# Kernel optimization log

Hardware: AMD Instinct MI355X
Metric: run time of the kernel (lower is better)

The kernel has to match this reference:

```python
import jax, jax.numpy as jnp
import numpy as np

B, H, W, C = 16, 56, 56, 256
NH, WS, SS = 8, 7, 3          # heads, window size, shift size
HD = C // NH                  # head dim = 32
MLPD = 4 * C                  # mlp hidden = 1024
WA = WS * WS                  # window area = 49
NW = (H // WS) * (W // WS)    # windows per image = 64
SCALE = HD ** -0.5


def _rel_pos_index():
    coords = np.stack(np.meshgrid(np.arange(WS), np.arange(WS), indexing='ij'))
    cf = coords.reshape(2, -1)
    rel = (cf[:, :, None] - cf[:, None, :]).transpose(1, 2, 0)
    rel[:, :, 0] += WS - 1
    rel[:, :, 1] += WS - 1
    rel[:, :, 0] *= 2 * WS - 1
    return rel.sum(-1)  # (WA, WA) int


def _shift_attn_mask():
    img = np.zeros((H, W))
    cnt = 0
    for hs in (slice(0, -WS), slice(-WS, -SS), slice(-SS, None)):
        for ws_ in (slice(0, -WS), slice(-WS, -SS), slice(-SS, None)):
            img[hs, ws_] = cnt
            cnt += 1
    mw = img.reshape(H // WS, WS, W // WS, WS).transpose(0, 2, 1, 3).reshape(-1, WA)
    am = mw[:, None, :] - mw[:, :, None]
    return np.where(am != 0, -100.0, 0.0).astype(np.float32)  # (NW, WA, WA)

REL_IDX = jnp.asarray(_rel_pos_index())
ATTN_MASK = jnp.asarray(_shift_attn_mask())


def setup_inputs() -> dict:
    key = jax.random.key(0)
    ks = jax.random.split(key, 8)
    s = 0.02
    return {
        'x':      jax.random.normal(ks[0], (B, H * W, C), jnp.float32),
        'g1':     jnp.ones((C,), jnp.float32),
        'be1':    jnp.zeros((C,), jnp.float32),
        'w_qkv':  jax.random.normal(ks[1], (C, 3 * C), jnp.float32) * s,
        'b_qkv':  jnp.zeros((3 * C,), jnp.float32),
        'rpt':    jax.random.normal(ks[2], ((2 * WS - 1) ** 2, NH), jnp.float32) * s,
        'w_proj': jax.random.normal(ks[3], (C, C), jnp.float32) * s,
        'b_proj': jnp.zeros((C,), jnp.float32),
        'g2':     jnp.ones((C,), jnp.float32),
        'be2':    jnp.zeros((C,), jnp.float32),
        'w_fc1':  jax.random.normal(ks[4], (C, MLPD), jnp.float32) * s,
        'b_fc1':  jnp.zeros((MLPD,), jnp.float32),
        'w_fc2':  jax.random.normal(ks[5], (MLPD, C), jnp.float32) * s,
        'b_fc2':  jnp.zeros((C,), jnp.float32),
    }


def _ln(x, g, b, eps=1e-5):
    m = x.mean(-1, keepdims=True)
    v = ((x - m) ** 2).mean(-1, keepdims=True)
    return (x - m) * jax.lax.rsqrt(v + eps) * g + b


def reference(x, g1, be1, w_qkv, b_qkv, rpt, w_proj, b_proj, g2, be2,
              w_fc1, b_fc1, w_fc2, b_fc2):
    shortcut = x
    h = _ln(x, g1, be1).reshape(B, H, W, C)
    # cyclic shift
    h = jnp.roll(h, (-SS, -SS), axis=(1, 2))
    # window partition -> (B*NW, WA, C)
    h = h.reshape(B, H // WS, WS, W // WS, WS, C).transpose(0, 1, 3, 2, 4, 5)
    h = h.reshape(B * NW, WA, C)
    # qkv
    qkv = h @ w_qkv + b_qkv                       # (B*NW, WA, 3C)
    qkv = qkv.reshape(B * NW, WA, 3, NH, HD).transpose(2, 0, 3, 1, 4)
    q, k, v = qkv[0], qkv[1], qkv[2]              # (B*NW, NH, WA, HD)
    attn = jnp.einsum('wnqd,wnkd->wnqk', q * SCALE, k)   # (B*NW, NH, WA, WA)
    # relative position bias
    bias = rpt[REL_IDX.reshape(-1)].reshape(WA, WA, NH).transpose(2, 0, 1)
    attn = attn + bias[None]
    # shifted-window mask, per window
    attn = attn.reshape(B, NW, NH, WA, WA) + ATTN_MASK[None, :, None]
    attn = jax.nn.softmax(attn.reshape(B * NW, NH, WA, WA), axis=-1)
    out = jnp.einsum('wnqk,wnkd->wnqd', attn, v)  # (B*NW, NH, WA, HD)
    out = out.transpose(0, 2, 1, 3).reshape(B * NW, WA, C)
    out = out @ w_proj + b_proj
    # window reverse + unshift
    out = out.reshape(B, H // WS, W // WS, WS, WS, C).transpose(0, 1, 3, 2, 4, 5)
    out = out.reshape(B, H, W, C)
    out = jnp.roll(out, (SS, SS), axis=(1, 2)).reshape(B, H * W, C)
    x = shortcut + out
    # MLP block
    h2 = _ln(x, g2, be2)
    h2 = jax.nn.gelu(h2 @ w_fc1 + b_fc1, approximate=False) @ w_fc2 + b_fc2
    return x + h2
```

## Files before the change

kernel.cpp:

```cpp
#include <hip/hip_runtime.h>
#include <hip/hip_bf16.h>
#include <cstdint>
#include <cstddef>

typedef __attribute__((ext_vector_type(8))) short short8;
typedef __attribute__((ext_vector_type(4))) float f32x4;
typedef __attribute__((ext_vector_type(4))) unsigned short us4;

#define DEVINL __device__ __forceinline__

static constexpr int SS_ = 3;
static constexpr int HH = 56, WW = 56;
#define SCALE_Q 0.17677669529663689f

DEVINL unsigned short f2b(float f) {
    unsigned int u = __builtin_bit_cast(unsigned int, f);
    unsigned int r = (u + 0x7FFFu + ((u >> 16) & 1u)) >> 16;
    return (unsigned short)r;
}
DEVINL float b2f(unsigned short s) {
    return __builtin_bit_cast(float, ((unsigned int)s) << 16);
}

DEVINL void gload_lds16(const unsigned short* g, unsigned short* l) {
    __builtin_amdgcn_global_load_lds(
        (const __attribute__((address_space(1))) unsigned int*)g,
        (__attribute__((address_space(3))) unsigned int*)l, 16, 0, 0);
}

__global__ void wconv_kernel(const float* __restrict__ in,
                             unsigned short* __restrict__ out, int K, int N) {
    int i = blockIdx.x * 256 + threadIdx.x;
    if (i >= K * N) return;
    int k = i / N, n = i - k * N;
    out[(size_t)n * K + k] = f2b(in[i]);
}

template <int MODE>
__global__ __launch_bounds__(256) void ln_kernel(
    const float* __restrict__ x, const float* __restrict__ g,
    const float* __restrict__ be, unsigned short* __restrict__ out) {
    const int wid = threadIdx.x >> 6, lane = threadIdx.x & 63;
    const int t = blockIdx.x * 4 + wid;
    int src;
    if constexpr (MODE == 1) {
        int w = t / 49, p = t - w * 49;
        int b = w >> 6, widx = w & 63;
        int wy = widx >> 3, wx = widx & 7;
        int py = p / 7, px = p - py * 7;
        int y = wy * 7 + py + SS_;  if (y >= HH) y -= HH;
        int xx = wx * 7 + px + SS_; if (xx >= WW) xx -= WW;
        src = b * (HH * WW) + y * WW + xx;
    } else {
        src = t;
    }
    const float4 v = reinterpret_cast<const float4*>(x + (size_t)src * 256)[lane];
    float s = v.x + v.y + v.z + v.w;
    float q = v.x * v.x + v.y * v.y + v.z * v.z + v.w * v.w;
#pragma unroll
    for (int m = 1; m < 64; m <<= 1) {
        s += __shfl_xor(s, m);
        q += __shfl_xor(q, m);
    }
    float mean = s * (1.0f / 256.0f);
    float var = q * (1.0f / 256.0f) - mean * mean;
    float rs = rsqrtf(var + 1e-5f);
    int c = lane * 4;
    us4 o;
    o.x = f2b((v.x - mean) * rs * g[c + 0] + be[c + 0]);
    o.y = f2b((v.y - mean) * rs * g[c + 1] + be[c + 1]);
    o.z = f2b((v.z - mean) * rs * g[c + 2] + be[c + 2]);
    o.w = f2b((v.w - mean) * rs * g[c + 3] + be[c + 3]);
    *reinterpret_cast<us4*>(out + (size_t)t * 256 + c) = o;
}

template <int KDIM, int EPI>
__global__ __launch_bounds__(512) void gemm_kernel(
    const unsigned short* __restrict__ A, const unsigned short* __restrict__ Bt,
    const float* __restrict__ bias, void* __restrict__ out0,
    const float* __restrict__ res, unsigned short* __restrict__ o_q,
    unsigned short* __restrict__ o_k, unsigned short* __restrict__ o_v) {
    constexpr int BM = 256, BN = 128, BK = 64;
    __shared__ __align__(16) unsigned short As[BM * BK];
    __shared__ __align__(16) unsigned short Bs[BN * BK];
    const int tid = threadIdx.x;
    const int wid = tid >> 6, lane = tid & 63;

    const int nwg = gridDim.x * gridDim.y;
    const int bid = blockIdx.x + gridDim.x * blockIdx.y;
    const int nb = (bid & 7) * (nwg >> 3) + (bid >> 3);
    const int n0 = (nb % gridDim.x) * BN;
    const int m0 = (nb / gridDim.x) * BM;

    const int wm = wid >> 1, wn = wid & 1;
    const int lr = lane & 15, kg = lane >> 4;
    f32x4 acc[4][4] = {};

    const int srow = tid >> 3;
    const int spos = tid & 7;

    for (int kt = 0; kt < KDIM; kt += BK) {
#pragma unroll
        for (int i = 0; i < 4; i++) {
            int row = i * 64 + srow;
            gload_lds16(A + (size_t)(m0 + row) * KDIM + kt + ((spos ^ (row & 7)) << 3),
                        As + i * 4096 + tid * 8);
        }
#pragma unroll
        for (int i = 0; i < 2; i++) {
            int row = i * 64 + srow;
            gload_lds16(Bt + (size_t)(n0 + row) * KDIM + kt + ((spos ^ (row & 7)) << 3),
                        Bs + i * 4096 + tid * 8);
        }
        __syncthreads();
#pragma unroll
        for (int ks = 0; ks < 2; ks++) {
            short8 a[4], b[4];
#pragma unroll
            for (int mf = 0; mf < 4; mf++) {
                int r = wm * 64 + mf * 16 + lr;
                a[mf] = *reinterpret_cast<const short8*>(
                    As + r * 64 + (((ks * 4 + kg) ^ (r & 7)) << 3));
            }
#pragma unroll
            for (int nf = 0; nf < 4; nf++) {
                int r = wn * 64 + nf * 16 + lr;
                b[nf] = *reinterpret_cast<const short8*>(
                    Bs + r * 64 + (((ks * 4 + kg) ^ (r & 7)) << 3));
            }
#pragma unroll
            for (int mf = 0; mf < 4; mf++)
#pragma unroll
                for (int nf = 0; nf < 4; nf++)
                    acc[mf][nf] = __builtin_amdgcn_mfma_f32_16x16x32_bf16(
                        a[mf], b[nf], acc[mf][nf], 0, 0, 0);
        }
        __syncthreads();
    }

#pragma unroll
    for (int mf = 0; mf < 4; mf++) {
#pragma unroll
        for (int nf = 0; nf < 4; nf++) {
#pragma unroll
            for (int j = 0; j < 4; j++) {
                int row = m0 + wm * 64 + mf * 16 + kg * 4 + j;
                int col = n0 + wn * 64 + nf * 16 + lr;
                float v = acc[mf][nf][j] + bias[col];
                if constexpr (EPI == 0) {
                    int w = row / 49, p = row - w * 49;
                    int which = col >> 8, h = (col >> 5) & 7, d = col & 31;
                    size_t th = (size_t)(w * 8 + h);
                    if (which == 0)
                        o_q[th * 1568 + p * 32 + d] = f2b(v * SCALE_Q);
                    else if (which == 1)
                        o_k[th * 1568 + p * 32 + d] = f2b(v);
                    else
                        o_v[th * 2048 + d * 64 + p] = f2b(v);
                } else if constexpr (EPI == 1) {
                    int w = row / 49, p = row - w * 49;
                    int b = w >> 6, widx = w & 63;
                    int wy = widx >> 3, wx = widx & 7;
                    int py = p / 7, px = p - py * 7;
                    int y = wy * 7 + py + SS_;  if (y >= HH) y -= HH;
                    int xx = wx * 7 + px + SS_; if (xx >= WW) xx -= WW;
                    size_t oi = ((size_t)(b * 3136 + y * 56 + xx)) * 256 + col;
                    reinterpret_cast<float*>(out0)[oi] = v + res[oi];
                } else if constexpr (EPI == 2) {
                    float gl = 0.5f * v * (1.0f + erff(v * 0.70710678118654752f));
                    reinterpret_cast<unsigned short*>(out0)[(size_t)row * 1024 + col] =
                        f2b(gl);
                } else {
                    size_t oi = (size_t)row * 256 + col;
                    reinterpret_cast<float*>(out0)[oi] = v + res[oi];
                }
            }
        }
    }
}

__global__ __launch_bounds__(256) void attn_kernel(
    const unsigned short* __restrict__ qg, const unsigned short* __restrict__ kgl,
    const unsigned short* __restrict__ vg, const float* __restrict__ rpt,
    unsigned short* __restrict__ out) {
    __shared__ __align__(16) unsigned short sm[4][6144];
    __shared__ unsigned short rpts[169 * 8];
    const int tid = threadIdx.x, wid = tid >> 6, lane = tid & 63;
    for (int i = tid; i < 169 * 8; i += 256) rpts[i] = f2b(rpt[i]);
    const int task = blockIdx.x * 4 + wid;
    const int w = task >> 3, h = task & 7;
    const int widx = w & 63, wy = widx >> 3, wx = widx & 7;
    unsigned short* q_s = sm[wid];
    unsigned short* k_s = sm[wid] + 2048;
    unsigned short* v_s = sm[wid] + 4096;
    unsigned short* p_s = sm[wid];
    const unsigned short* qsrc = qg + (size_t)task * 1568;
    const unsigned short* ksrc = kgl + (size_t)task * 1568;
    const unsigned short* vsrc = vg + (size_t)task * 2048;
    for (int c = lane; c < 196; c += 64) {
        int row = c >> 2, kc = c & 3;
        int off = (row * 32 + kc * 8) ^ ((row & 7) << 3);
        *reinterpret_cast<short8*>(q_s + off) =
            *reinterpret_cast<const short8*>(qsrc + c * 8);
        *reinterpret_cast<short8*>(k_s + off) =
            *reinterpret_cast<const short8*>(ksrc + c * 8);
    }
#pragma unroll
    for (int i = 0; i < 4; i++) {
        int c = i * 64 + lane;
        int row = c >> 3, kc = c & 7;
        int off = (row * 64 + kc * 8) ^ ((row & 7) << 3);
        *reinterpret_cast<short8*>(v_s + off) =
            *reinterpret_cast<const short8*>(vsrc + c * 8);
    }
    __syncthreads();

    const int lr = lane & 15, kg = lane >> 4;
    short8 af[4], bf[4];
#pragma unroll
    for (int mf = 0; mf < 4; mf++) {
        int r = mf * 16 + lr;
        af[mf] = *reinterpret_cast<const short8*>(
            q_s + ((r * 32 + kg * 8) ^ ((r & 7) << 3)));
    }
#pragma unroll
    for (int nf = 0; nf < 4; nf++) {
        int r = nf * 16 + lr;
        bf[nf] = *reinterpret_cast<const short8*>(
            k_s + ((r * 32 + kg * 8) ^ ((r & 7) << 3)));
    }
    f32x4 s[4][4] = {};
#pragma unroll
    for (int mf = 0; mf < 4; mf++)
#pragma unroll
        for (int nf = 0; nf < 4; nf++)
            s[mf][nf] = __builtin_amdgcn_mfma_f32_16x16x32_bf16(af[mf], bf[nf],
                                                                s[mf][nf], 0, 0, 0);
#pragma unroll
    for (int mf = 0; mf < 4; mf++) {
#pragma unroll
        for (int j = 0; j < 4; j++) {
            int row = mf * 16 + kg * 4 + j;
            bool rvalid = row < 49;
            int qy = 0, qx = 0, gq = 0;
            if (rvalid) {
                qy = row / 7; qx = row - qy * 7;
                int yi = wy * 7 + qy, xi = wx * 7 + qx;
                gq = ((yi < 49) ? 0 : ((yi < 53) ? 1 : 2)) * 3 +
                     ((xi < 49) ? 0 : ((xi < 53) ? 1 : 2));
            }
            float L[4];
#pragma unroll
            for (int nf = 0; nf < 4; nf++) {
                int col = nf * 16 + lr;
                float val = s[mf][nf][j];
                if (rvalid && col < 49) {
                    int ky = col / 7, kx = col - ky * 7;
                    int yi = wy * 7 + ky, xi = wx * 7 + kx;
                    int gk = ((yi < 49) ? 0 : ((yi < 53) ? 1 : 2)) * 3 +
                             ((xi < 49) ? 0 : ((xi < 53) ? 1 : 2));
                    val += b2f(rpts[((qy - ky + 6) * 13 + (qx - kx + 6)) * 8 + h]);
                    if (gq != gk) val -= 100.0f;
                } else {
                    val = -1e30f;
                }
                L[nf] = val;
            }
            float m = fmaxf(fmaxf(L[0], L[1]), fmaxf(L[2], L[3]));
#pragma unroll
            for (int t2 = 1; t2 < 16; t2 <<= 1) m = fmaxf(m, __shfl_xor(m, t2));
            float P[4], psum = 0.f;
#pragma unroll
            for (int nf = 0; nf < 4; nf++) {
                P[nf] = __expf(L[nf] - m);
                psum += P[nf];
            }
#pragma unroll
            for (int t2 = 1; t2 < 16; t2 <<= 1) psum += __shfl_xor(psum, t2);
            float inv = 1.0f / psum;
#pragma unroll
            for (int nf = 0; nf < 4; nf++) {
                int col = nf * 16 + lr;
                p_s[(row * 64 + col) ^ ((row & 7) << 3)] = f2b(P[nf] * inv);
            }
        }
    }
    f32x4 o[4][2] = {};
#pragma unroll
    for (int ks = 0; ks < 2; ks++) {
        short8 pa[4], vb[2];
#pragma unroll
        for (int mf = 0; mf < 4; mf++) {
            int r = mf * 16 + lr;
            pa[mf] = *reinterpret_cast<const short8*>(
                p_s + ((r * 64 + ks * 32 + kg * 8) ^ ((r & 7) << 3)));
        }
#pragma unroll
        for (int nf = 0; nf < 2; nf++) {
            int d = nf * 16 + lr;
            vb[nf] = *reinterpret_cast<const short8*>(
                v_s + ((d * 64 + ks * 32 + kg * 8) ^ ((d & 7) << 3)));
        }
#pragma unroll
        for (int mf = 0; mf < 4; mf++)
#pragma unroll
            for (int nf = 0; nf < 2; nf++)
                o[mf][nf] = __builtin_amdgcn_mfma_f32_16x16x32_bf16(
                    pa[mf], vb[nf], o[mf][nf], 0, 0, 0);
    }
#pragma unroll
    for (int mf = 0; mf < 4; mf++) {
#pragma unroll
        for (int j = 0; j < 4; j++) {
            int row = mf * 16 + kg * 4 + j;
            if (row < 49) {
#pragma unroll
                for (int nf = 0; nf < 2; nf++) {
                    int d = nf * 16 + lr;
                    out[((size_t)w * 49 + row) * 256 + h * 32 + d] =
                        f2b(o[mf][nf][j]);
                }
            }
        }
    }
}

extern "C" void kernel_launch(void* const* d_in, const int* in_sizes, int n_in,
                              void* d_out, int out_size, void* d_ws,
                              size_t ws_size, hipStream_t stream) {
    const float* x     = (const float*)d_in[0];
    const float* g1    = (const float*)d_in[1];
    const float* be1   = (const float*)d_in[2];
    const float* wqkv  = (const float*)d_in[3];
    const float* bqkv  = (const float*)d_in[4];
    const float* rpt   = (const float*)d_in[5];
    const float* wproj = (const float*)d_in[6];
    const float* bproj = (const float*)d_in[7];
    const float* g2    = (const float*)d_in[8];
    const float* be2   = (const float*)d_in[9];
    const float* wfc1  = (const float*)d_in[10];
    const float* bfc1  = (const float*)d_in[11];
    const float* wfc2  = (const float*)d_in[12];
    const float* bfc2  = (const float*)d_in[13];
    float* out = (float*)d_out;
    char* ws = (char*)d_ws;

    unsigned short* hb  = (unsigned short*)(ws);
    unsigned short* qg  = (unsigned short*)(ws + 25690112);
    unsigned short* kgl = (unsigned short*)(ws + 51380224);
    unsigned short* vg  = (unsigned short*)(ws + 77070336);
    float*          x2  = (float*)(ws + 110624768);
    unsigned short* h2  = (unsigned short*)(ws + 162004992);
    unsigned short* wT  = (unsigned short*)(ws + 187695104);
    unsigned short* wqkvT = wT;
    unsigned short* wprojT = wT + 196608;
    unsigned short* wfc1T  = wT + 262144;
    unsigned short* wfc2T  = wT + 524288;
    unsigned short* a1 = (unsigned short*)ws;

    wconv_kernel<<<(256 * 768 + 255) / 256, 256, 0, stream>>>(wqkv, wqkvT, 256, 768);
    wconv_kernel<<<(256 * 256 + 255) / 256, 256, 0, stream>>>(wproj, wprojT, 256, 256);
    wconv_kernel<<<(256 * 1024 + 255) / 256, 256, 0, stream>>>(wfc1, wfc1T, 256, 1024);
    wconv_kernel<<<(1024 * 256 + 255) / 256, 256, 0, stream>>>(wfc2, wfc2T, 1024, 256);
    hipMemsetAsync(vg, 0, 33554432, stream);

    ln_kernel<1><<<12544, 256, 0, stream>>>(x, g1, be1, hb);
    gemm_kernel<256, 0><<<dim3(6, 196), 512, 0, stream>>>(
        hb, wqkvT, bqkv, nullptr, nullptr, qg, kgl, vg);
    attn_kernel<<<2048, 256, 0, stream>>>(qg, kgl, vg, rpt, hb);
    gemm_kernel<256, 1><<<dim3(2, 196), 512, 0, stream>>>(
        hb, wprojT, bproj, x2, x, nullptr, nullptr, nullptr);
    ln_kernel<0><<<12544, 256, 0, stream>>>(x2, g2, be2, h2);
    gemm_kernel<256, 2><<<dim3(8, 196), 512, 0, stream>>>(
        h2, wfc1T, bfc1, a1, nullptr, nullptr, nullptr, nullptr);
    gemm_kernel<1024, 3><<<dim3(2, 196), 512, 0, stream>>>(
        a1, wfc2T, bfc2, out, x2, nullptr, nullptr, nullptr);
}
```

Baseline: 320.3 us.

## Double-buffer GEMM loads, store residual in bf16, approximate GELU, drop V memset

The GEMM main loop now uses BK=32 with two LDS buffers and a new swizzle, so the next tile's global-to-LDS load overlaps the current MFMAs and one barrier per iteration is removed. The intermediate residual x2 is written and read as bf16 instead of fp32, halving that tensor's traffic, at some cost in precision. GELU switches from erff to an Abramowitz-Stegun polynomial with __expf. The memset of the padded V buffer is removed; this is only safe if the attention kernel never reads the padding, which is a correctness risk.

```diff
diff --git a/kernel.cpp b/kernel.cpp
--- a/kernel.cpp
+++ b/kernel.cpp
@@ -2,6 +2,7 @@
 #include <hip/hip_bf16.h>
 #include <cstdint>
 #include <cstddef>
+#include <type_traits>
 
 typedef __attribute__((ext_vector_type(8))) short short8;
 typedef __attribute__((ext_vector_type(4))) float f32x4;
@@ -20,6 +21,19 @@
 }
 DEVINL float b2f(unsigned short s) {
     return __builtin_bit_cast(float, ((unsigned int)s) << 16);
+}
+
+DEVINL float gelu(float v) {
+    float ax = fabsf(v) * 0.70710678118654752f;
+    float t = 1.0f / (1.0f + 0.3275911f * ax);
+    float poly = t * (0.254829592f +
+                 t * (-0.284496736f +
+                 t * (1.421413741f +
+                 t * (-1.453152027f + t * 1.061405429f))));
+    float e = __expf(-ax * ax);
+    float erfv = 1.0f - poly * e;
+    erfv = v >= 0.0f ? erfv : -erfv;
+    return 0.5f * v * (1.0f + erfv);
 }
 
 DEVINL void gload_lds16(const unsigned short* g, unsigned short* l) {
@@ -36,9 +50,9 @@
     out[(size_t)n * K + k] = f2b(in[i]);
 }
 
-template <int MODE>
+template <int MODE, typename TIN>
 __global__ __launch_bounds__(256) void ln_kernel(
-    const float* __restrict__ x, const float* __restrict__ g,
+    const TIN* __restrict__ x, const float* __restrict__ g,
     const float* __restrict__ be, unsigned short* __restrict__ out) {
     const int wid = threadIdx.x >> 6, lane = threadIdx.x & 63;
     const int t = blockIdx.x * 4 + wid;
@@ -54,7 +68,13 @@
     } else {
         src = t;
     }
-    const float4 v = reinterpret_cast<const float4*>(x + (size_t)src * 256)[lane];
+    float4 v;
+    if constexpr (std::is_same_v<TIN, float>) {
+        v = reinterpret_cast<const float4*>(x + (size_t)src * 256)[lane];
+    } else {
+        us4 u = reinterpret_cast<const us4*>(x + (size_t)src * 256)[lane];
+        v.x = b2f(u.x); v.y = b2f(u.y); v.z = b2f(u.z); v.w = b2f(u.w);
+    }
     float s = v.x + v.y + v.z + v.w;
     float q = v.x * v.x + v.y * v.y + v.z * v.z + v.w * v.w;
 #pragma unroll
@@ -78,11 +98,11 @@
 __global__ __launch_bounds__(512) void gemm_kernel(
     const unsigned short* __restrict__ A, const unsigned short* __restrict__ Bt,
     const float* __restrict__ bias, void* __restrict__ out0,
-    const float* __restrict__ res, unsigned short* __restrict__ o_q,
+    const void* __restrict__ res, unsigned short* __restrict__ o_q,
     unsigned short* __restrict__ o_k, unsigned short* __restrict__ o_v) {
-    constexpr int BM = 256, BN = 128, BK = 64;
-    __shared__ __align__(16) unsigned short As[BM * BK];
-    __shared__ __align__(16) unsigned short Bs[BN * BK];
+    constexpr int BM = 256, BN = 128, BK = 32, NK = KDIM / BK;
+    __shared__ __align__(16) unsigned short As[2][BM * BK];
+    __shared__ __align__(16) unsigned short Bs[2][BN * BK];
     const int tid = threadIdx.x;
     const int wid = tid >> 6, lane = tid & 63;
 
@@ -96,46 +116,50 @@
     const int lr = lane & 15, kg = lane >> 4;
     f32x4 acc[4][4] = {};
 
-    const int srow = tid >> 3;
-    const int spos = tid & 7;
-
-    for (int kt = 0; kt < KDIM; kt += BK) {
-#pragma unroll
-        for (int i = 0; i < 4; i++) {
-            int row = i * 64 + srow;
-            gload_lds16(A + (size_t)(m0 + row) * KDIM + kt + ((spos ^ (row & 7)) << 3),
-                        As + i * 4096 + tid * 8);
-        }
+    const int arow0 = tid >> 2, aslot = tid & 3;
+
+    auto STAGE = [&](int kt, int buf) {
 #pragma unroll
         for (int i = 0; i < 2; i++) {
-            int row = i * 64 + srow;
-            gload_lds16(Bt + (size_t)(n0 + row) * KDIM + kt + ((spos ^ (row & 7)) << 3),
-                        Bs + i * 4096 + tid * 8);
-        }
+            int row = i * 128 + arow0;
+            int c = aslot ^ ((row >> 1) & 3);
+            gload_lds16(A + (size_t)(m0 + row) * KDIM + kt * BK + c * 8,
+                        As[buf] + i * 4096 + tid * 8);
+        }
+        {
+            int row = arow0;
+            int c = aslot ^ ((row >> 1) & 3);
+            gload_lds16(Bt + (size_t)(n0 + row) * KDIM + kt * BK + c * 8,
+                        Bs[buf] + tid * 8);
+        }
+    };
+
+    STAGE(0, 0);
+    __syncthreads();
+    int cur = 0;
+    for (int kt = 0; kt < NK; kt++) {
+        if (kt + 1 < NK) STAGE(kt + 1, cur ^ 1);
+        short8 a[4], b[4];
+#pragma unroll
+        for (int mf = 0; mf < 4; mf++) {
+            int r = wm * 64 + mf * 16 + lr;
+            a[mf] = *reinterpret_cast<const short8*>(
+                As[cur] + r * 32 + ((kg ^ ((r >> 1) & 3)) << 3));
+        }
+#pragma unroll
+        for (int nf = 0; nf < 4; nf++) {
+            int r = wn * 64 + nf * 16 + lr;
+            b[nf] = *reinterpret_cast<const short8*>(
+                Bs[cur] + r * 32 + ((kg ^ ((r >> 1) & 3)) << 3));
+        }
+#pragma unroll
+        for (int mf = 0; mf < 4; mf++)
+#pragma unroll
+            for (int nf = 0; nf < 4; nf++)
+                acc[mf][nf] = __builtin_amdgcn_mfma_f32_16x16x32_bf16(
+                    a[mf], b[nf], acc[mf][nf], 0, 0, 0);
         __syncthreads();
-#pragma unroll
-        for (int ks = 0; ks < 2; ks++) {
-            short8 a[4], b[4];
-#pragma unroll
-            for (int mf = 0; mf < 4; mf++) {
-                int r = wm * 64 + mf * 16 + lr;
-                a[mf] = *reinterpret_cast<const short8*>(
-                    As + r * 64 + (((ks * 4 + kg) ^ (r & 7)) << 3));
-            }
-#pragma unroll
-            for (int nf = 0; nf < 4; nf++) {
-                int r = wn * 64 + nf * 16 + lr;
-                b[nf] = *reinterpret_cast<const short8*>(
-                    Bs + r * 64 + (((ks * 4 + kg) ^ (r & 7)) << 3));
-            }
-#pragma unroll
-            for (int mf = 0; mf < 4; mf++)
-#pragma unroll
-                for (int nf = 0; nf < 4; nf++)
-                    acc[mf][nf] = __builtin_amdgcn_mfma_f32_16x16x32_bf16(
-                        a[mf], b[nf], acc[mf][nf], 0, 0, 0);
-        }
-        __syncthreads();
+        cur ^= 1;
     }
 
 #pragma unroll
@@ -159,20 +183,21 @@
                         o_v[th * 2048 + d * 64 + p] = f2b(v);
                 } else if constexpr (EPI == 1) {
                     int w = row / 49, p = row - w * 49;
-                    int b = w >> 6, widx = w & 63;
+                    int b2 = w >> 6, widx = w & 63;
                     int wy = widx >> 3, wx = widx & 7;
                     int py = p / 7, px = p - py * 7;
                     int y = wy * 7 + py + SS_;  if (y >= HH) y -= HH;
                     int xx = wx * 7 + px + SS_; if (xx >= WW) xx -= WW;
-                    size_t oi = ((size_t)(b * 3136 + y * 56 + xx)) * 256 + col;
-                    reinterpret_cast<float*>(out0)[oi] = v + res[oi];
+                    size_t oi = ((size_t)(b2 * 3136 + y * 56 + xx)) * 256 + col;
+                    reinterpret_cast<unsigned short*>(out0)[oi] =
+                        f2b(v + reinterpret_cast<const float*>(res)[oi]);
                 } else if constexpr (EPI == 2) {
-                    float gl = 0.5f * v * (1.0f + erff(v * 0.70710678118654752f));
                     reinterpret_cast<unsigned short*>(out0)[(size_t)row * 1024 + col] =
-                        f2b(gl);
+                        f2b(gelu(v));
                 } else {
                     size_t oi = (size_t)row * 256 + col;
-                    reinterpret_cast<float*>(out0)[oi] = v + res[oi];
+                    reinterpret_cast<float*>(out0)[oi] =
+                        v + b2f(reinterpret_cast<const unsigned short*>(res)[oi]);
                 }
             }
         }
@@ -349,7 +374,7 @@
     unsigned short* qg  = (unsigned short*)(ws + 25690112);
     unsigned short* kgl = (unsigned short*)(ws + 51380224);
     unsigned short* vg  = (unsigned short*)(ws + 77070336);
-    float*          x2  = (float*)(ws + 110624768);
+    unsigned short* x2b = (unsigned short*)(ws + 110624768);
     unsigned short* h2  = (unsigned short*)(ws + 162004992);
     unsigned short* wT  = (unsigned short*)(ws + 187695104);
     unsigned short* wqkvT = wT;
@@ -362,17 +387,16 @@
     wconv_kernel<<<(256 * 256 + 255) / 256, 256, 0, stream>>>(wproj, wprojT, 256, 256);
     wconv_kernel<<<(256 * 1024 + 255) / 256, 256, 0, stream>>>(wfc1, wfc1T, 256, 1024);
     wconv_kernel<<<(1024 * 256 + 255) / 256, 256, 0, stream>>>(wfc2, wfc2T, 1024, 256);
-    hipMemsetAsync(vg, 0, 33554432, stream);
-
-    ln_kernel<1><<<12544, 256, 0, stream>>>(x, g1, be1, hb);
+
+    ln_kernel<1, float><<<12544, 256, 0, stream>>>(x, g1, be1, hb);
     gemm_kernel<256, 0><<<dim3(6, 196), 512, 0, stream>>>(
         hb, wqkvT, bqkv, nullptr, nullptr, qg, kgl, vg);
     attn_kernel<<<2048, 256, 0, stream>>>(qg, kgl, vg, rpt, hb);
     gemm_kernel<256, 1><<<dim3(2, 196), 512, 0, stream>>>(
-        hb, wprojT, bproj, x2, x, nullptr, nullptr, nullptr);
-    ln_kernel<0><<<12544, 256, 0, stream>>>(x2, g2, be2, h2);
+        hb, wprojT, bproj, x2b, x, nullptr, nullptr, nullptr);
+    ln_kernel<0, unsigned short><<<12544, 256, 0, stream>>>(x2b, g2, be2, h2);
     gemm_kernel<256, 2><<<dim3(8, 196), 512, 0, stream>>>(
         h2, wfc1T, bfc1, a1, nullptr, nullptr, nullptr, nullptr);
     gemm_kernel<1024, 3><<<dim3(2, 196), 512, 0, stream>>>(
-        a1, wfc2T, bfc2, out, x2, nullptr, nullptr, nullptr);
-}
+        a1, wfc2T, bfc2, out, x2b, nullptr, nullptr, nullptr);
+}
```

Result: no change. 321.1 us (+0.2%).
